# Kernel optimization log

Measured on AMD Instinct MI355X. Metric: run time of the kernel, lower is better.

## Reference

```python
import jax, jax.numpy as jnp
import numpy as np

BATCH, SEQ, DIN, FILTERS, KSIZE = 64, 512, 256, 256, 3

def setup_inputs() -> dict:
    key = jax.random.key(0)
    ks = jax.random.split(key, 5)
    s_u = 1.0 / np.sqrt(DIN)
    return {
        "x": jax.random.normal(ks[0], (BATCH, SEQ, DIN), dtype=jnp.float32),
        "z": jax.random.normal(ks[1], (BATCH, DIN), dtype=jnp.float32),
        "U": jax.random.normal(ks[2], (DIN, DIN), dtype=jnp.float32) * s_u,
        "V": jax.random.normal(ks[3], (DIN, KSIZE * FILTERS), dtype=jnp.float32) * s_u,
        "B_w": jax.random.normal(ks[4], (DIN, KSIZE * FILTERS), dtype=jnp.float32) * s_u,
        "b": jnp.zeros((FILTERS,), dtype=jnp.float32),
        "kernel_size": KSIZE,
    }

def reference(x, z, U, V, B_w, b, kernel_size):
    Bn, L, din = x.shape
    K = int(kernel_size)
    F = V.shape[1] // K
    # per-sample dynamic kernel: (U * sigmoid(z)) @ V + B
    zf = jax.nn.sigmoid(z)                                  # (B, din)
    f = jnp.einsum('de,be,ef->bdf', U, zf, V) + B_w[None]    # (B, din, K*F)
    f = f.reshape(Bn, din, K, F).transpose(0, 2, 1, 3)       # (B, K, din, F)
    # 'same' padding, stride 1
    pad_l, pad_r = (K - 1) // 2, K // 2
    xp = jnp.pad(x, ((0, 0), (pad_l, pad_r), (0, 0)))        # (B, L+K-1, din)
    patches = jnp.stack([xp[:, i:i + L] for i in range(K)], axis=2)  # (B, L, K, din)
    out = jnp.einsum('blkd,bkdf->blf', patches, f) + b       # (B, L, F)
    return jax.nn.relu(out)
```

## Files before the change

kernel.cpp:

```cpp
#include <hip/hip_runtime.h>
#include <math.h>

#define BATCH 64
#define SEQL  512
#define DIN   256
#define NF    256
#define KS    3
#define KF    (KS * NF)

#define XCH 512
#define KC  (KS * XCH)
#define PR2 66
#define PLD 128
#define P0SZ (PR2 * PLD)

typedef __attribute__((ext_vector_type(8))) short short8;
typedef __attribute__((ext_vector_type(4))) float floatx4;
typedef __attribute__((ext_vector_type(16))) float floatx16;
typedef __attribute__((ext_vector_type(8))) unsigned short ushort8v;
typedef __attribute__((ext_vector_type(4))) unsigned short ushort4v;

static __device__ __forceinline__ unsigned short f2bf(float f) {
    unsigned int u = __float_as_uint(f);
    return (unsigned short)((u + 0x7FFF + ((u >> 16) & 1)) >> 16);
}

static __device__ __forceinline__ void gl_lds16(const void* g, void* l) {
    __builtin_amdgcn_global_load_lds(
        (const __attribute__((address_space(1))) unsigned int*)g,
        (__attribute__((address_space(3))) unsigned int*)l, 16, 0, 0);
}

__global__ __launch_bounds__(256) void pack_kernel(
    const float* __restrict__ U, const float* __restrict__ V,
    const float* __restrict__ Bw,
    unsigned short* __restrict__ WcT, unsigned short* __restrict__ UT)
{
    const int blk = blockIdx.x;
    const int t   = threadIdx.x;
    __shared__ unsigned short tile[64][64 + 2];

    if (blk < 96) {
        const int f0 = (blk & 3) * 64, c0 = (blk >> 2) * 64;
        const int fl = t & 63, cb = t >> 6;
        #pragma unroll
        for (int it = 0; it < 16; ++it) {
            const int cl = cb + it * 4;
            const int c  = c0 + cl;
            const int k  = c >> 9, ch = c & (XCH - 1);
            const float v = (ch < DIN) ? Bw[(size_t)ch * KF + k * NF + f0 + fl]
                                       : V[(size_t)(ch - DIN) * KF + k * NF + f0 + fl];
            tile[cl][fl] = f2bf(v);
        }
        __syncthreads();
        const int cl2 = t & 63, fb = t >> 6;
        #pragma unroll
        for (int it = 0; it < 16; ++it) {
            const int fl2 = fb + it * 4;
            WcT[(size_t)(f0 + fl2) * KC + c0 + cl2] = tile[cl2][fl2];
        }
    } else {
        const int bb = blk - 96;
        const int e0 = (bb & 3) * 64, d0 = (bb >> 2) * 64;
        const int el = t & 63, db = t >> 6;
        #pragma unroll
        for (int it = 0; it < 16; ++it) {
            const int dl = db + it * 4;
            tile[dl][el] = f2bf(U[(size_t)(d0 + dl) * DIN + e0 + el]);
        }
        __syncthreads();
        const int dl2 = t & 63, eb = t >> 6;
        #pragma unroll
        for (int it = 0; it < 16; ++it) {
            const int el2 = eb + it * 4;
            UT[(size_t)(e0 + el2) * DIN + d0 + dl2] = tile[dl2][el2];
        }
    }
}

__global__ __launch_bounds__(256, 2) void fused_kernel(
    const float* __restrict__ x, const float* __restrict__ z,
    const unsigned short* __restrict__ UT,
    const unsigned short* __restrict__ WcT,
    const float* __restrict__ bias, float* __restrict__ out)
{
    __shared__ __align__(16) unsigned short lds[2 * P0SZ + 2 * 8192];
    unsigned short* P0 = lds;
    unsigned short* P1 = lds + P0SZ;
    unsigned short* Bs = lds + 2 * P0SZ;

    const int tid  = threadIdx.x;
    const int lane = tid & 63;
    const int wave = tid >> 6;
    const int quad = lane >> 4, l16 = lane & 15;
    const int l32  = lane & 31, hi  = lane >> 5;
    const int r4   = lane >> 2, ud4 = lane & 3;

    const int bid = blockIdx.x;
    const int b   = bid >> 3;
    const int l0  = (bid & 7) * 64;

    floatx16 acc2[2][2] = {};
    floatx4  accY[4][5] = {};

    auto stage32 = [&](const unsigned short* gbase, size_t rs,
                       unsigned short* buf) {
        #pragma unroll
        for (int c = 0; c < 4; ++c) {
            const int rr = wave * 64 + c * 16 + r4;
            gl_lds16(gbase + (size_t)rr * rs + ((ud4 ^ (rr & 3)) << 3),
                     buf + (size_t)(wave * 64 + c * 16) * 32);
        }
    };
    auto stageB = [&](int r) {
        const int g = r / 12, k = (r / 4) % 3, hq = r & 3;
        stage32(WcT + (size_t)k * XCH + g * 128 + hq * 32, KC,
                Bs + (size_t)(r & 1) * 8192);
    };
    auto stageU = [&](int kk) {
        stage32(UT + (size_t)kk * 32, DIN, Bs + (size_t)(kk & 1) * 8192);
    };

    auto convRegion = [&](int r) {
        const unsigned short* buf = Bs + (size_t)(r & 1) * 8192;
        const int g = r / 12, k = (r / 4) % 3, hq = r & 3;
        const unsigned short* P = (g & 1) ? P1 : P0;
        __builtin_amdgcn_s_setprio(1);
        #pragma unroll
        for (int ks = 0; ks < 2; ++ks) {
            short8 af[2], bf[2];
            const int ua = hq * 4 + ks * 2 + hi;
            #pragma unroll
            for (int i = 0; i < 2; ++i) {
                const int m = i * 32 + l32 + k;
                af[i] = *(const short8*)&P[m * PLD + ((ua ^ (m & 15)) << 3)];
            }
            const int ub = ks * 2 + hi;
            #pragma unroll
            for (int j = 0; j < 2; ++j) {
                const int n = wave * 64 + j * 32 + l32;
                bf[j] = *(const short8*)&buf[n * 32 + ((ub ^ (n & 3)) << 3)];
            }
            #pragma unroll
            for (int i = 0; i < 2; ++i)
                #pragma unroll
                for (int j = 0; j < 2; ++j)
                    acc2[i][j] = __builtin_amdgcn_mfma_f32_32x32x16_bf16(
                        af[i], bf[j], acc2[i][j], 0, 0, 0);
        }
        __builtin_amdgcn_s_setprio(0);
    };

    auto gChunk = [&](int kk) {
        const unsigned short* buf = Bs + (size_t)(kk & 1) * 8192;
        const unsigned short* P = (kk >= 4) ? P1 : P0;
        const int ux = (kk & 3) * 4 + quad;
        __builtin_amdgcn_s_setprio(1);
        short8 uf[4];
        #pragma unroll
        for (int q = 0; q < 4; ++q) {
            const int n = q * 64 + wave * 16 + l16;
            uf[q] = *(const short8*)&buf[n * 32 + ((quad ^ (n & 3)) << 3)];
        }
        #pragma unroll
        for (int i = 0; i < 5; ++i) {
            const int row = i * 16 + l16;
            const short8 xf = *(const short8*)
                &P[row * PLD + ((ux ^ (row & 15)) << 3)];
            #pragma unroll
            for (int q = 0; q < 4; ++q)
                accY[q][i] = __builtin_amdgcn_mfma_f32_16x16x32_bf16(
                    uf[q], xf, accY[q][i], 0, 0, 0);
        }
        __builtin_amdgcn_s_setprio(0);
    };

    auto yEpi = [&](int eh) {
        unsigned short* PY = eh ? P1 : P0;
        #pragma unroll
        for (int q2 = 0; q2 < 2; ++q2) {
            const int q  = eh * 2 + q2;
            const int e0 = (q * 4 + wave) * 16 + quad * 4;
            const int c0 = e0 & 127;
            float zf[4];
            #pragma unroll
            for (int r2 = 0; r2 < 4; ++r2)
                zf[r2] = 1.0f / (1.0f + expf(-z[(size_t)b * DIN + e0 + r2]));
            const int u = c0 >> 3;
            #pragma unroll
            for (int i = 0; i < 5; ++i) {
                const int xrow = i * 16 + l16;
                if (xrow < PR2) {
                    ushort4v h;
                    #pragma unroll
                    for (int r2 = 0; r2 < 4; ++r2)
                        h[r2] = f2bf(accY[q][i][r2] * zf[r2]);
                    *(ushort4v*)&PY[xrow * PLD + ((u ^ (xrow & 15)) << 3) +
                                    (c0 & 7)] = h;
                }
            }
        }
    };

    #pragma unroll
    for (int p = 0; p < 2; ++p) {
        unsigned short* P = p ? P1 : P0;
        #pragma unroll
        for (int it = 0; it < 5; ++it) {
            const int idx = tid + it * 256;
            if (idx < PR2 * 16) {
                const int row = idx >> 4, u = idx & 15;
                const int l = l0 - 1 + row;
                ushort8v h = {};
                if (l >= 0 && l < SEQL) {
                    const float* xp =
                        x + ((size_t)b * SEQL + l) * DIN + p * 128 + u * 8;
                    const float4 v0 = *(const float4*)xp;
                    const float4 v1 = *(const float4*)(xp + 4);
                    h[0] = f2bf(v0.x); h[1] = f2bf(v0.y);
                    h[2] = f2bf(v0.z); h[3] = f2bf(v0.w);
                    h[4] = f2bf(v1.x); h[5] = f2bf(v1.y);
                    h[6] = f2bf(v1.z); h[7] = f2bf(v1.w);
                }
                *(ushort8v*)&P[row * PLD + ((u ^ (row & 15)) << 3)] = h;
            }
        }
    }

    stageU(0);
    __syncthreads();
    #pragma unroll 1
    for (int kk = 0; kk < 8; ++kk) {
        if (kk < 7) stageU(kk + 1); else stageB(0);
        gChunk(kk);
        __syncthreads();
    }

    #pragma unroll 1
    for (int r = 0; r < 12; ++r) { stageB(r + 1); convRegion(r); __syncthreads(); }
    yEpi(0);

    #pragma unroll 1
    for (int r = 12; r < 24; ++r) { stageB(r + 1); convRegion(r); __syncthreads(); }
    yEpi(1);

    #pragma unroll 1
    for (int r = 24; r < 48; ++r) {
        if (r < 47) stageB(r + 1);
        convRegion(r);
        __syncthreads();
    }

    #pragma unroll
    for (int j = 0; j < 2; ++j) {
        const int f  = wave * 64 + j * 32 + l32;
        const float bv = bias[f];
        #pragma unroll
        for (int i = 0; i < 2; ++i) {
            #pragma unroll
            for (int reg = 0; reg < 16; ++reg) {
                const int rowl = i * 32 + (reg & 3) + 8 * (reg >> 2) + 4 * hi;
                const float v = acc2[i][j][reg] + bv;
                out[((size_t)b * SEQL + l0 + rowl) * NF + f] = fmaxf(v, 0.0f);
            }
        }
    }
}

extern "C" void kernel_launch(void* const* d_in, const int* in_sizes, int n_in,
                              void* d_out, int out_size, void* d_ws, size_t ws_size,
                              hipStream_t stream) {
    const float* x    = (const float*)d_in[0];
    const float* z    = (const float*)d_in[1];
    const float* U    = (const float*)d_in[2];
    const float* V    = (const float*)d_in[3];
    const float* Bw   = (const float*)d_in[4];
    const float* bias = (const float*)d_in[5];

    unsigned short* WcT = (unsigned short*)d_ws;
    unsigned short* UT  = WcT + (size_t)NF * KC;
    float* out = (float*)d_out;

    pack_kernel<<<dim3(112), 256, 0, stream>>>(U, V, Bw, WcT, UT);
    fused_kernel<<<dim3(512), 256, 0, stream>>>(x, z, UT, WcT, bias, out);
}
```

Baseline: 136.9 us.

## Load weight fragments directly from global memory instead of LDS staging

```diff
diff --git a/kernel.cpp b/kernel.cpp
--- a/kernel.cpp
+++ b/kernel.cpp
@@ -23,12 +23,6 @@
 static __device__ __forceinline__ unsigned short f2bf(float f) {
     unsigned int u = __float_as_uint(f);
     return (unsigned short)((u + 0x7FFF + ((u >> 16) & 1)) >> 16);
-}
-
-static __device__ __forceinline__ void gl_lds16(const void* g, void* l) {
-    __builtin_amdgcn_global_load_lds(
-        (const __attribute__((address_space(1))) unsigned int*)g,
-        (__attribute__((address_space(3))) unsigned int*)l, 16, 0, 0);
 }
 
 __global__ __launch_bounds__(256) void pack_kernel(
@@ -84,127 +78,21 @@
     const unsigned short* __restrict__ WcT,
     const float* __restrict__ bias, float* __restrict__ out)
 {
-    __shared__ __align__(16) unsigned short lds[2 * P0SZ + 2 * 8192];
-    unsigned short* P0 = lds;
-    unsigned short* P1 = lds + P0SZ;
-    unsigned short* Bs = lds + 2 * P0SZ;
+    __shared__ __align__(16) unsigned short lds[4 * P0SZ];
 
     const int tid  = threadIdx.x;
     const int lane = tid & 63;
     const int wave = tid >> 6;
     const int quad = lane >> 4, l16 = lane & 15;
     const int l32  = lane & 31, hi  = lane >> 5;
-    const int r4   = lane >> 2, ud4 = lane & 3;
 
     const int bid = blockIdx.x;
     const int b   = bid >> 3;
     const int l0  = (bid & 7) * 64;
 
-    floatx16 acc2[2][2] = {};
-    floatx4  accY[4][5] = {};
-
-    auto stage32 = [&](const unsigned short* gbase, size_t rs,
-                       unsigned short* buf) {
-        #pragma unroll
-        for (int c = 0; c < 4; ++c) {
-            const int rr = wave * 64 + c * 16 + r4;
-            gl_lds16(gbase + (size_t)rr * rs + ((ud4 ^ (rr & 3)) << 3),
-                     buf + (size_t)(wave * 64 + c * 16) * 32);
-        }
-    };
-    auto stageB = [&](int r) {
-        const int g = r / 12, k = (r / 4) % 3, hq = r & 3;
-        stage32(WcT + (size_t)k * XCH + g * 128 + hq * 32, KC,
-                Bs + (size_t)(r & 1) * 8192);
-    };
-    auto stageU = [&](int kk) {
-        stage32(UT + (size_t)kk * 32, DIN, Bs + (size_t)(kk & 1) * 8192);
-    };
-
-    auto convRegion = [&](int r) {
-        const unsigned short* buf = Bs + (size_t)(r & 1) * 8192;
-        const int g = r / 12, k = (r / 4) % 3, hq = r & 3;
-        const unsigned short* P = (g & 1) ? P1 : P0;
-        __builtin_amdgcn_s_setprio(1);
-        #pragma unroll
-        for (int ks = 0; ks < 2; ++ks) {
-            short8 af[2], bf[2];
-            const int ua = hq * 4 + ks * 2 + hi;
-            #pragma unroll
-            for (int i = 0; i < 2; ++i) {
-                const int m = i * 32 + l32 + k;
-                af[i] = *(const short8*)&P[m * PLD + ((ua ^ (m & 15)) << 3)];
-            }
-            const int ub = ks * 2 + hi;
-            #pragma unroll
-            for (int j = 0; j < 2; ++j) {
-                const int n = wave * 64 + j * 32 + l32;
-                bf[j] = *(const short8*)&buf[n * 32 + ((ub ^ (n & 3)) << 3)];
-            }
-            #pragma unroll
-            for (int i = 0; i < 2; ++i)
-                #pragma unroll
-                for (int j = 0; j < 2; ++j)
-                    acc2[i][j] = __builtin_amdgcn_mfma_f32_32x32x16_bf16(
-                        af[i], bf[j], acc2[i][j], 0, 0, 0);
-        }
-        __builtin_amdgcn_s_setprio(0);
-    };
-
-    auto gChunk = [&](int kk) {
-        const unsigned short* buf = Bs + (size_t)(kk & 1) * 8192;
-        const unsigned short* P = (kk >= 4) ? P1 : P0;
-        const int ux = (kk & 3) * 4 + quad;
-        __builtin_amdgcn_s_setprio(1);
-        short8 uf[4];
-        #pragma unroll
-        for (int q = 0; q < 4; ++q) {
-            const int n = q * 64 + wave * 16 + l16;
-            uf[q] = *(const short8*)&buf[n * 32 + ((quad ^ (n & 3)) << 3)];
-        }
-        #pragma unroll
-        for (int i = 0; i < 5; ++i) {
-            const int row = i * 16 + l16;
-            const short8 xf = *(const short8*)
-                &P[row * PLD + ((ux ^ (row & 15)) << 3)];
-            #pragma unroll
-            for (int q = 0; q < 4; ++q)
-                accY[q][i] = __builtin_amdgcn_mfma_f32_16x16x32_bf16(
-                    uf[q], xf, accY[q][i], 0, 0, 0);
-        }
-        __builtin_amdgcn_s_setprio(0);
-    };
-
-    auto yEpi = [&](int eh) {
-        unsigned short* PY = eh ? P1 : P0;
-        #pragma unroll
-        for (int q2 = 0; q2 < 2; ++q2) {
-            const int q  = eh * 2 + q2;
-            const int e0 = (q * 4 + wave) * 16 + quad * 4;
-            const int c0 = e0 & 127;
-            float zf[4];
-            #pragma unroll
-            for (int r2 = 0; r2 < 4; ++r2)
-                zf[r2] = 1.0f / (1.0f + expf(-z[(size_t)b * DIN + e0 + r2]));
-            const int u = c0 >> 3;
-            #pragma unroll
-            for (int i = 0; i < 5; ++i) {
-                const int xrow = i * 16 + l16;
-                if (xrow < PR2) {
-                    ushort4v h;
-                    #pragma unroll
-                    for (int r2 = 0; r2 < 4; ++r2)
-                        h[r2] = f2bf(accY[q][i][r2] * zf[r2]);
-                    *(ushort4v*)&PY[xrow * PLD + ((u ^ (xrow & 15)) << 3) +
-                                    (c0 & 7)] = h;
-                }
-            }
-        }
-    };
-
     #pragma unroll
     for (int p = 0; p < 2; ++p) {
-        unsigned short* P = p ? P1 : P0;
+        unsigned short* P = lds + (size_t)p * P0SZ;
         #pragma unroll
         for (int it = 0; it < 5; ++it) {
             const int idx = tid + it * 256;
@@ -226,29 +114,89 @@
             }
         }
     }
-
-    stageU(0);
     __syncthreads();
+
+    {
+        floatx4 accY[4][5] = {};
+        #pragma unroll 1
+        for (int kk = 0; kk < 8; ++kk) {
+            const unsigned short* P = lds + (size_t)(kk >> 2) * P0SZ;
+            const int ux = (kk & 3) * 4 + quad;
+            short8 uf[4];
+            #pragma unroll
+            for (int q = 0; q < 4; ++q) {
+                const int e = q * 64 + wave * 16 + l16;
+                uf[q] = *(const short8*)
+                    &UT[(size_t)e * DIN + kk * 32 + quad * 8];
+            }
+            #pragma unroll
+            for (int i = 0; i < 5; ++i) {
+                const int row = i * 16 + l16;
+                const short8 xf = *(const short8*)
+                    &P[row * PLD + ((ux ^ (row & 15)) << 3)];
+                #pragma unroll
+                for (int q = 0; q < 4; ++q)
+                    accY[q][i] = __builtin_amdgcn_mfma_f32_16x16x32_bf16(
+                        uf[q], xf, accY[q][i], 0, 0, 0);
+            }
+        }
+        #pragma unroll
+        for (int q = 0; q < 4; ++q) {
+            const int e0 = q * 64 + wave * 16 + quad * 4;
+            unsigned short* PY = lds + (size_t)(2 + (q >> 1)) * P0SZ;
+            const int c0 = e0 & 127;
+            float zf[4];
+            #pragma unroll
+            for (int r2 = 0; r2 < 4; ++r2)
+                zf[r2] = 1.0f / (1.0f + expf(-z[(size_t)b * DIN + e0 + r2]));
+            const int u = c0 >> 3;
+            #pragma unroll
+            for (int i = 0; i < 5; ++i) {
+                const int xrow = i * 16 + l16;
+                if (xrow < PR2) {
+                    ushort4v h;
+                    #pragma unroll
+                    for (int r2 = 0; r2 < 4; ++r2)
+                        h[r2] = f2bf(accY[q][i][r2] * zf[r2]);
+                    *(ushort4v*)&PY[xrow * PLD + ((u ^ (xrow & 15)) << 3) +
+                                    (c0 & 7)] = h;
+                }
+            }
+        }
+    }
+    __syncthreads();
+
+    floatx16 acc2[2][2] = {};
     #pragma unroll 1
-    for (int kk = 0; kk < 8; ++kk) {
-        if (kk < 7) stageU(kk + 1); else stageB(0);
-        gChunk(kk);
-        __syncthreads();
-    }
-
-    #pragma unroll 1
-    for (int r = 0; r < 12; ++r) { stageB(r + 1); convRegion(r); __syncthreads(); }
-    yEpi(0);
-
-    #pragma unroll 1
-    for (int r = 12; r < 24; ++r) { stageB(r + 1); convRegion(r); __syncthreads(); }
-    yEpi(1);
-
-    #pragma unroll 1
-    for (int r = 24; r < 48; ++r) {
-        if (r < 47) stageB(r + 1);
-        convRegion(r);
-        __syncthreads();
+    for (int g = 0; g < 4; ++g) {
+        const unsigned short* P = lds + (size_t)g * P0SZ;
+        #pragma unroll 1
+        for (int k = 0; k < KS; ++k) {
+            const unsigned short* gW = WcT + (size_t)k * XCH + g * 128;
+            #pragma unroll
+            for (int ks = 0; ks < 8; ++ks) {
+                short8 af[2], bf[2];
+                const int ua = ks * 2 + hi;
+                #pragma unroll
+                for (int i = 0; i < 2; ++i) {
+                    const int m = i * 32 + l32 + k;
+                    af[i] = *(const short8*)
+                        &P[m * PLD + ((ua ^ (m & 15)) << 3)];
+                }
+                #pragma unroll
+                for (int j = 0; j < 2; ++j) {
+                    const int f = wave * 64 + j * 32 + l32;
+                    bf[j] = *(const short8*)
+                        &gW[(size_t)f * KC + ks * 16 + hi * 8];
+                }
+                #pragma unroll
+                for (int i = 0; i < 2; ++i)
+                    #pragma unroll
+                    for (int j = 0; j < 2; ++j)
+                        acc2[i][j] = __builtin_amdgcn_mfma_f32_32x32x16_bf16(
+                            af[i], bf[j], acc2[i][j], 0, 0, 0);
+            }
+        }
     }
 
     #pragma unroll
```

Measured after the change: 155.8 us. 13.8% more time.
